# Kernel tuning notes

Hardware: AMD Instinct MI355X
Metric: run time of the kernel (lower is better)

Reference implementation:

```python
import jax, jax.numpy as jnp
import numpy as np

H = 16      # attention heads
D = 1024    # embedding size
HD = 64     # head size = D // H


def setup_inputs() -> dict:
    key = jax.random.key(0)
    ks = jax.random.split(key, 6)
    s = 1.0 / np.sqrt(D)
    x = jax.random.normal(ks[0], (2, 2048, D), dtype=jnp.float32)
    Wq = jax.random.normal(ks[1], (H, D, HD), dtype=jnp.float32) * s
    Wk = jax.random.normal(ks[2], (H, D, HD), dtype=jnp.float32) * s
    Wv = jax.random.normal(ks[3], (H, D, HD), dtype=jnp.float32) * s
    Wo = jax.random.normal(ks[4], (H * HD, D), dtype=jnp.float32) * s
    bo = jax.random.normal(ks[5], (D,), dtype=jnp.float32) * 0.01
    return {"x": x, "Wq": Wq, "Wk": Wk, "Wv": Wv, "Wo": Wo, "bo": bo}


def reference(x, Wq, Wk, Wv, Wo, bo):
    # x: [B, S, D]; per-head projections batched over the head axis.
    B, S, _ = x.shape
    q = jnp.einsum('bsd,hde->bhse', x, Wq)  # [B,H,S,HD]
    k = jnp.einsum('bsd,hde->bhse', x, Wk)
    v = jnp.einsum('bsd,hde->bhse', x, Wv)
    scale = 1.0 / jnp.sqrt(jnp.asarray(HD, dtype=x.dtype))
    scores = jnp.einsum('bhqe,bhke->bhqk', q, k) * scale  # [B,H,S,S]
    causal = jnp.tril(jnp.ones((S, S), dtype=bool))
    scores = jnp.where(causal, scores, jnp.asarray(-jnp.inf, dtype=x.dtype))
    attn = jax.nn.softmax(scores, axis=-1)
    out = jnp.einsum('bhqk,bhke->bhqe', attn, v)  # [B,H,S,HD]
    # concat heads along last dim (head order matches ModuleList order)
    out = out.transpose(0, 2, 1, 3).reshape(B, S, H * HD)
    return out @ Wo + bo  # dropout is identity in eval mode
```

## Files before the change

kernel.cpp:

```cpp
#include <hip/hip_runtime.h>
#include <hip/hip_bf16.h>
#include <cstdint>

#define Hh 16
#define Dd 1024
#define HD 64
#define Bb 2
#define Ss 2048

typedef float f32x4 __attribute__((ext_vector_type(4)));
typedef __bf16 bf16x8 __attribute__((ext_vector_type(8)));

__device__ __forceinline__ unsigned short f2bf(float f) {
  union { float f; unsigned u; } v; v.f = f;
  unsigned r = (v.u + 0x7FFFu + ((v.u >> 16) & 1u)) >> 16;
  return (unsigned short)r;
}

__device__ __forceinline__ void gld16(const void* g, void* l) {
  __builtin_amdgcn_global_load_lds(
      (__attribute__((address_space(1))) void*)(g),
      (__attribute__((address_space(3))) void*)(l),
      16, 0, 0);
}

__global__ __launch_bounds__(256)
void pack_x_k(const float4* __restrict__ x, unsigned short* __restrict__ xb, int n4) {
  const int i = blockIdx.x * blockDim.x + threadIdx.x;
  if (i >= n4) return;
  const float4 v = x[i];
  ushort4 o;
  o.x = f2bf(v.x); o.y = f2bf(v.y); o.z = f2bf(v.z); o.w = f2bf(v.w);
  *(ushort4*)&xb[(size_t)i * 4] = o;
}

__global__ __launch_bounds__(256)
void tconv_k(const float* __restrict__ in, unsigned short* __restrict__ out,
             int R, int C, float scale) {
  __shared__ float T[64][65];
  const int m = blockIdx.z;
  const float* src = in + (size_t)m * R * C;
  unsigned short* dst = out + (size_t)m * R * C;
  const int c0 = blockIdx.x * 64, r0 = blockIdx.y * 64;
  const int tx = threadIdx.x & 63, ty = threadIdx.x >> 6;
#pragma unroll
  for (int it = 0; it < 16; ++it) {
    const int i = ty + it * 4;
    T[i][tx] = src[(size_t)(r0 + i) * C + c0 + tx];
  }
  __syncthreads();
#pragma unroll
  for (int it = 0; it < 16; ++it) {
    const int jj = ty + it * 4;
    dst[(size_t)(c0 + jj) * R + r0 + tx] = f2bf(T[tx][jj] * scale);
  }
}

template <int EPI>
__global__ __launch_bounds__(256)
void gemm_bt(const unsigned short* __restrict__ A,
             const unsigned short* __restrict__ Bt,
             int K, int Ndim,
             unsigned short* __restrict__ q_out,
             unsigned short* __restrict__ k_out,
             unsigned short* __restrict__ vt_out,
             float* __restrict__ o_out,
             const float* __restrict__ bias)
{
  __shared__ unsigned short As[2][128 * 64];
  __shared__ unsigned short Bs[2][128 * 64];

  const int tid = threadIdx.x;
  const int w = tid >> 6, lane = tid & 63;
  const int lo = lane & 15, hi = lane >> 4;
  const int wr = w >> 1, wc = w & 1;
  const int row0 = blockIdx.y * 128;
  const int col0 = blockIdx.x * 128;

  f32x4 acc[4][4] = {};

  const int srow = w * 32 + (lane >> 3);
  const int scol = ((lane & 7) ^ (lane >> 3)) * 8;
  const int swl  = (lo & 7) << 4;

#define GSTAGE(bi, k0)                                                    \
  _Pragma("unroll")                                                       \
  for (int c = 0; c < 4; ++c) {                                           \
    const int rr = srow + c * 8;                                          \
    gld16(A  + (size_t)(row0 + rr) * K + ((k0) + scol),                   \
          (char*)&As[bi][0] + (w * 4 + c) * 1024);                        \
    gld16(Bt + (size_t)(col0 + rr) * K + ((k0) + scol),                   \
          (char*)&Bs[bi][0] + (w * 4 + c) * 1024);                        \
  }

  GSTAGE(0, 0);
  __syncthreads();

  const int nst = K >> 6;
  int cur = 0;
  for (int t = 0; t < nst; ++t) {
    if (t + 1 < nst) { GSTAGE(cur ^ 1, (t + 1) * 64); }
#pragma unroll
    for (int ks = 0; ks < 2; ++ks) {
      bf16x8 af[4], bfr[4];
#pragma unroll
      for (int i = 0; i < 4; ++i)
        af[i] = *(const bf16x8*)((const char*)&As[cur][0] +
                 (wr * 64 + i * 16 + lo) * 128 + ((ks * 64 + hi * 16) ^ swl));
#pragma unroll
      for (int j = 0; j < 4; ++j)
        bfr[j] = *(const bf16x8*)((const char*)&Bs[cur][0] +
                 (wc * 64 + j * 16 + lo) * 128 + ((ks * 64 + hi * 16) ^ swl));
      __builtin_amdgcn_s_setprio(1);
#pragma unroll
      for (int i = 0; i < 4; ++i)
#pragma unroll
        for (int j = 0; j < 4; ++j) {
          if (EPI == 1)
            acc[i][j] = __builtin_amdgcn_mfma_f32_16x16x32_bf16(af[i], bfr[j], acc[i][j], 0, 0, 0);
          else
            acc[i][j] = __builtin_amdgcn_mfma_f32_16x16x32_bf16(bfr[j], af[i], acc[i][j], 0, 0, 0);
        }
      __builtin_amdgcn_s_setprio(0);
    }
    __syncthreads();
    cur ^= 1;
  }

#pragma unroll
  for (int i = 0; i < 4; ++i) {
#pragma unroll
    for (int j = 0; j < 4; ++j) {
      if (EPI == 1) {
        const int grow = row0 + wr * 64 + i * 16 + hi * 4;
        const int gcol = col0 + wc * 64 + j * 16 + lo;
        const int hd = gcol >> 6, e = gcol & 63;
        const int bb2 = grow >> 11, s = grow & 2047;
        ushort4 pk;
        pk.x = f2bf(acc[i][j][0]); pk.y = f2bf(acc[i][j][1]);
        pk.z = f2bf(acc[i][j][2]); pk.w = f2bf(acc[i][j][3]);
        *(ushort4*)&vt_out[((size_t)(bb2 * Hh + hd) * HD + e) * Ss + s] = pk;
      } else {
        const int m  = row0 + wr * 64 + i * 16 + lo;
        const int n0 = col0 + wc * 64 + j * 16 + hi * 4;
        if (EPI == 0) {
          const int p = n0 >> 10;
          const int hd = (n0 >> 6) & 15;
          const int e = n0 & 63;
          const int bb2 = m >> 11, s = m & 2047;
          unsigned short* dst = (p == 0) ? q_out : k_out;
          ushort4 pk;
          pk.x = f2bf(acc[i][j][0]); pk.y = f2bf(acc[i][j][1]);
          pk.z = f2bf(acc[i][j][2]); pk.w = f2bf(acc[i][j][3]);
          *(ushort4*)&dst[((size_t)(bb2 * Hh + hd) * Ss + s) * HD + e] = pk;
        } else {
          const float4 bv = *(const float4*)&bias[n0];
          float4 o;
          o.x = acc[i][j][0] + bv.x; o.y = acc[i][j][1] + bv.y;
          o.z = acc[i][j][2] + bv.z; o.w = acc[i][j][3] + bv.w;
          *(float4*)&o_out[(size_t)m * Ndim + n0] = o;
        }
      }
    }
  }
#undef GSTAGE
}

__global__ __launch_bounds__(256)
void attn_fwd(const unsigned short* __restrict__ qb,
              const unsigned short* __restrict__ kb,
              const unsigned short* __restrict__ vtb,
              unsigned short* __restrict__ ob)
{
  __shared__ unsigned short Ks[2][64 * 64];
  __shared__ unsigned short Vs[2][64 * 64];
  __shared__ unsigned short Ps[4][16 * 64];

  const int qt = 31 - blockIdx.y;
  const int bh = blockIdx.x;
  const int bb2 = bh >> 4;
  const int hd = bh & 15;

  const unsigned short* Q  = qb  + (size_t)bh * Ss * HD;
  const unsigned short* Kg = kb  + (size_t)bh * Ss * HD;
  const unsigned short* Vt = vtb + (size_t)bh * HD * Ss;

  const int tid = threadIdx.x;
  const int w = tid >> 6, lane = tid & 63;
  const int lo = lane & 15, hi = lane >> 4;
  const int qrow0 = qt * 64 + w * 16;

  const int srow = lane >> 3;
  const int scol = ((lane & 7) ^ (lane >> 3)) * 8;

#define STAGE(bi, kv)                                                     \
  _Pragma("unroll")                                                       \
  for (int c = 0; c < 2; ++c) {                                           \
    const int L = c * 4 + w;                                              \
    const int rr = L * 8 + srow;                                          \
    gld16(Kg + (size_t)((kv) + rr) * HD + scol,                           \
          (char*)&Ks[bi][0] + L * 1024);                                  \
    gld16(Vt + (size_t)rr * Ss + (kv) + scol,                             \
          (char*)&Vs[bi][0] + L * 1024);                                  \
  }

  const int swl = (lo & 7) << 4;

  bf16x8 vones;
#pragma unroll
  for (int j = 0; j < 8; ++j) vones[j] = (__bf16)1.0f;

  bf16x8 qf[2];
#pragma unroll
  for (int ks = 0; ks < 2; ++ks)
    qf[ks] = *(const bf16x8*)&Q[(size_t)(qrow0 + lo) * HD + ks * 32 + hi * 8];

  f32x4 oacc[4] = {};
  float m2[4], l2[4];
#pragma unroll
  for (int r = 0; r < 4; ++r) { m2[r] = -INFINITY; l2[r] = 0.f; }

  const int ntiles = qt + 1;

  STAGE(0, 0);
  __syncthreads();

  int cur = 0;
  for (int t = 0; t < ntiles; ++t) {
    if (t + 1 < ntiles) { STAGE(cur ^ 1, (t + 1) * 64); }

    const int kv0 = t * 64;
    const bool diag = (t == qt);

    f32x4 sacc[4] = {};
    __builtin_amdgcn_s_setprio(1);
#pragma unroll
    for (int ks = 0; ks < 2; ++ks) {
      bf16x8 kf[4];
#pragma unroll
      for (int nj = 0; nj < 4; ++nj)
        kf[nj] = *(const bf16x8*)((const char*)&Ks[cur][0] +
                 (nj * 16 + lo) * 128 + ((ks * 64 + hi * 16) ^ swl));
#pragma unroll
      for (int nj = 0; nj < 4; ++nj)
        sacc[nj] = __builtin_amdgcn_mfma_f32_16x16x32_bf16(qf[ks], kf[nj], sacc[nj], 0, 0, 0);
    }
    __builtin_amdgcn_s_setprio(0);

    float lm[4];
    float dmax = -INFINITY;
#pragma unroll
    for (int r = 0; r < 4; ++r) {
      if (diag) {
        const int q = qrow0 + hi * 4 + r;
#pragma unroll
        for (int nj = 0; nj < 4; ++nj) {
          const int kk = kv0 + nj * 16 + lo;
          if (kk > q) sacc[nj][r] = -INFINITY;
        }
      }
      lm[r] = fmaxf(fmaxf(sacc[0][r], sacc[1][r]), fmaxf(sacc[2][r], sacc[3][r]));
      dmax = fmaxf(dmax, lm[r] - m2[r]);
    }
    if (!__all(dmax <= 8.0f)) {
#pragma unroll
      for (int r = 0; r < 4; ++r) {
        float rm = lm[r];
#pragma unroll
        for (int d = 1; d < 16; d <<= 1)
          rm = fmaxf(rm, __shfl_xor(rm, d, 64));
        const float mn = fmaxf(m2[r], rm);
        const float rc = __builtin_amdgcn_exp2f(m2[r] - mn);
        m2[r] = mn;
        l2[r] *= rc;
#pragma unroll
        for (int nj = 0; nj < 4; ++nj)
          oacc[nj][r] *= rc;
      }
    }

    unsigned short* Pw = &Ps[w][0];
#pragma unroll
    for (int nj = 0; nj < 4; ++nj)
#pragma unroll
      for (int r = 0; r < 4; ++r) {
        const float p = __builtin_amdgcn_exp2f(sacc[nj][r] - m2[r]);
        const int prow = hi * 4 + r;
        const int pcb = (nj * 32 + lo * 2) ^ ((prow & 7) << 4);
        *(__bf16*)((char*)Pw + prow * 128 + pcb) = (__bf16)p;
      }

    f32x4 osum = {};
    __builtin_amdgcn_s_setprio(1);
#pragma unroll
    for (int ks = 0; ks < 2; ++ks) {
      bf16x8 pa, vf[4];
      pa = *(const bf16x8*)((const char*)Pw +
           lo * 128 + ((ks * 64 + hi * 16) ^ swl));
#pragma unroll
      for (int nj = 0; nj < 4; ++nj)
        vf[nj] = *(const bf16x8*)((const char*)&Vs[cur][0] +
                 (nj * 16 + lo) * 128 + ((ks * 64 + hi * 16) ^ swl));
#pragma unroll
      for (int nj = 0; nj < 4; ++nj)
        oacc[nj] = __builtin_amdgcn_mfma_f32_16x16x32_bf16(pa, vf[nj], oacc[nj], 0, 0, 0);
      osum = __builtin_amdgcn_mfma_f32_16x16x32_bf16(pa, vones, osum, 0, 0, 0);
    }
    __builtin_amdgcn_s_setprio(0);
#pragma unroll
    for (int r = 0; r < 4; ++r)
      l2[r] += osum[r];

    __syncthreads();
    cur ^= 1;
  }
#undef STAGE

#pragma unroll
  for (int r = 0; r < 4; ++r) {
    const int s = qrow0 + hi * 4 + r;
    const float il = 1.0f / l2[r];
    const size_t base = ((size_t)bb2 * Ss + s) * Dd + hd * HD;
#pragma unroll
    for (int nj = 0; nj < 4; ++nj)
      ob[base + nj * 16 + lo] = f2bf(oacc[nj][r] * il);
  }
}

extern "C" void kernel_launch(void* const* d_in, const int* in_sizes, int n_in,
                              void* d_out, int out_size, void* d_ws, size_t ws_size,
                              hipStream_t stream)
{
  const float* x  = (const float*)d_in[0];
  const float* Wq = (const float*)d_in[1];
  const float* Wk = (const float*)d_in[2];
  const float* Wv = (const float*)d_in[3];
  const float* Wo = (const float*)d_in[4];
  const float* bo = (const float*)d_in[5];
  float* out = (float*)d_out;

  char* ws = (char*)d_ws;
  unsigned short* xb    = (unsigned short*)(ws);
  unsigned short* wqkvT = (unsigned short*)(ws + 8388608);
  unsigned short* woT   = (unsigned short*)(ws + 14680064);
  unsigned short* qb    = (unsigned short*)(ws + 16777216);
  unsigned short* kb    = (unsigned short*)(ws + 25165824);
  unsigned short* vtb   = (unsigned short*)(ws + 33554432);
  unsigned short* ob    = (unsigned short*)(ws + 41943040);

  pack_x_k<<<4096, 256, 0, stream>>>((const float4*)x, xb, 1048576);
  tconv_k<<<dim3(1, 16, 16), 256, 0, stream>>>(Wq, wqkvT,           1024, 64, 0.18033688011112042f);
  tconv_k<<<dim3(1, 16, 16), 256, 0, stream>>>(Wk, wqkvT + 1048576, 1024, 64, 1.0f);
  tconv_k<<<dim3(1, 16, 16), 256, 0, stream>>>(Wv, wqkvT + 2097152, 1024, 64, 1.0f);
  tconv_k<<<dim3(16, 16, 1), 256, 0, stream>>>(Wo, woT,             1024, 1024, 1.0f);

  gemm_bt<0><<<dim3(16, 32), 256, 0, stream>>>(xb, wqkvT, 1024, 0,
                                               qb, kb, nullptr, nullptr, nullptr);
  gemm_bt<1><<<dim3(8, 32), 256, 0, stream>>>(xb, wqkvT + 2097152, 1024, 0,
                                              nullptr, nullptr, vtb, nullptr, nullptr);
  attn_fwd<<<dim3(32, 32), 256, 0, stream>>>(qb, kb, vtb, ob);
  gemm_bt<2><<<dim3(8, 32), 256, 0, stream>>>(ob, woT, 1024, 1024,
                                              nullptr, nullptr, nullptr, out, bo);
}
```

Before: 131.0 us.

## Keep attention probabilities in registers and give each wave 32 query rows

```diff
diff --git a/kernel.cpp b/kernel.cpp
--- a/kernel.cpp
+++ b/kernel.cpp
@@ -166,7 +166,7 @@
 #undef GSTAGE
 }
 
-__global__ __launch_bounds__(256)
+__global__ __launch_bounds__(128)
 void attn_fwd(const unsigned short* __restrict__ qb,
               const unsigned short* __restrict__ kb,
               const unsigned short* __restrict__ vtb,
@@ -174,7 +174,6 @@
 {
   __shared__ unsigned short Ks[2][64 * 64];
   __shared__ unsigned short Vs[2][64 * 64];
-  __shared__ unsigned short Ps[4][16 * 64];
 
   const int qt = 31 - blockIdx.y;
   const int bh = blockIdx.x;
@@ -188,19 +187,24 @@
   const int tid = threadIdx.x;
   const int w = tid >> 6, lane = tid & 63;
   const int lo = lane & 15, hi = lane >> 4;
-  const int qrow0 = qt * 64 + w * 16;
-
-  const int srow = lane >> 3;
-  const int scol = ((lane & 7) ^ (lane >> 3)) * 8;
+  const int qrow0 = qt * 64 + w * 32;
+
+  const int sr  = lane >> 3;
+  const int scol = ((lane & 7) ^ sr) * 8;
+  int prow[4];
+#pragma unroll
+  for (int c = 0; c < 4; ++c) {
+    const int L = c * 2 + w;
+    prow[c] = (L >> 2) * 32 + ((L & 1) * 2 + (sr >> 2)) * 8 + ((L >> 1) & 1) * 4 + (sr & 3);
+  }
 
 #define STAGE(bi, kv)                                                     \
   _Pragma("unroll")                                                       \
-  for (int c = 0; c < 2; ++c) {                                           \
-    const int L = c * 4 + w;                                              \
-    const int rr = L * 8 + srow;                                          \
-    gld16(Kg + (size_t)((kv) + rr) * HD + scol,                           \
+  for (int c = 0; c < 4; ++c) {                                           \
+    const int L = c * 2 + w;                                              \
+    gld16(Kg + (size_t)((kv) + prow[c]) * HD + scol,                      \
           (char*)&Ks[bi][0] + L * 1024);                                  \
-    gld16(Vt + (size_t)rr * Ss + (kv) + scol,                             \
+    gld16(Vt + (size_t)(L * 8 + sr) * Ss + (kv) + scol,                   \
           (char*)&Vs[bi][0] + L * 1024);                                  \
   }
 
@@ -210,15 +214,22 @@
 #pragma unroll
   for (int j = 0; j < 8; ++j) vones[j] = (__bf16)1.0f;
 
-  bf16x8 qf[2];
-#pragma unroll
-  for (int ks = 0; ks < 2; ++ks)
-    qf[ks] = *(const bf16x8*)&Q[(size_t)(qrow0 + lo) * HD + ks * 32 + hi * 8];
-
-  f32x4 oacc[4] = {};
-  float m2[4], l2[4];
-#pragma unroll
-  for (int r = 0; r < 4; ++r) { m2[r] = -INFINITY; l2[r] = 0.f; }
+  bf16x8 qf[2][2];
+#pragma unroll
+  for (int mi = 0; mi < 2; ++mi)
+#pragma unroll
+    for (int ks = 0; ks < 2; ++ks)
+      qf[mi][ks] = *(const bf16x8*)&Q[(size_t)(qrow0 + mi * 16 + lo) * HD + ks * 32 + hi * 8];
+
+  f32x4 oacc[2][4] = {};
+  float m2s[2];
+  float l2[2][4];
+#pragma unroll
+  for (int mi = 0; mi < 2; ++mi) {
+    m2s[mi] = -INFINITY;
+#pragma unroll
+    for (int r = 0; r < 4; ++r) l2[mi][r] = 0.f;
+  }
 
   const int ntiles = qt + 1;
 
@@ -229,10 +240,7 @@
   for (int t = 0; t < ntiles; ++t) {
     if (t + 1 < ntiles) { STAGE(cur ^ 1, (t + 1) * 64); }
 
-    const int kv0 = t * 64;
-    const bool diag = (t == qt);
-
-    f32x4 sacc[4] = {};
+    f32x4 sacc[2][4] = {};
     __builtin_amdgcn_s_setprio(1);
 #pragma unroll
     for (int ks = 0; ks < 2; ++ks) {
@@ -242,74 +250,98 @@
         kf[nj] = *(const bf16x8*)((const char*)&Ks[cur][0] +
                  (nj * 16 + lo) * 128 + ((ks * 64 + hi * 16) ^ swl));
 #pragma unroll
-      for (int nj = 0; nj < 4; ++nj)
-        sacc[nj] = __builtin_amdgcn_mfma_f32_16x16x32_bf16(qf[ks], kf[nj], sacc[nj], 0, 0, 0);
+      for (int mi = 0; mi < 2; ++mi)
+#pragma unroll
+        for (int nj = 0; nj < 4; ++nj)
+          sacc[mi][nj] = __builtin_amdgcn_mfma_f32_16x16x32_bf16(kf[nj], qf[mi][ks], sacc[mi][nj], 0, 0, 0);
     }
     __builtin_amdgcn_s_setprio(0);
 
-    float lm[4];
-    float dmax = -INFINITY;
-#pragma unroll
-    for (int r = 0; r < 4; ++r) {
-      if (diag) {
-        const int q = qrow0 + hi * 4 + r;
+    if (t == qt) {
+#pragma unroll
+      for (int mi = 0; mi < 2; ++mi) {
+        const int qr = w * 32 + mi * 16 + lo;
 #pragma unroll
         for (int nj = 0; nj < 4; ++nj) {
-          const int kk = kv0 + nj * 16 + lo;
-          if (kk > q) sacc[nj][r] = -INFINITY;
+          const int kb0 = (nj >> 1) * 32 + (nj & 1) * 4 + hi * 8;
+#pragma unroll
+          for (int r = 0; r < 4; ++r)
+            if (kb0 + r > qr) sacc[mi][nj][r] = -INFINITY;
         }
       }
-      lm[r] = fmaxf(fmaxf(sacc[0][r], sacc[1][r]), fmaxf(sacc[2][r], sacc[3][r]));
-      dmax = fmaxf(dmax, lm[r] - m2[r]);
-    }
+    }
+
+    float lmax[2];
+#pragma unroll
+    for (int mi = 0; mi < 2; ++mi) {
+      float a = fmaxf(fmaxf(sacc[mi][0][0], sacc[mi][0][1]),
+                      fmaxf(sacc[mi][0][2], sacc[mi][0][3]));
+      float b = fmaxf(fmaxf(sacc[mi][1][0], sacc[mi][1][1]),
+                      fmaxf(sacc[mi][1][2], sacc[mi][1][3]));
+      float c = fmaxf(fmaxf(sacc[mi][2][0], sacc[mi][2][1]),
+                      fmaxf(sacc[mi][2][2], sacc[mi][2][3]));
+      float d = fmaxf(fmaxf(sacc[mi][3][0], sacc[mi][3][1]),
+                      fmaxf(sacc[mi][3][2], sacc[mi][3][3]));
+      lmax[mi] = fmaxf(fmaxf(a, b), fmaxf(c, d));
+    }
+    const float dmax = fmaxf(lmax[0] - m2s[0], lmax[1] - m2s[1]);
     if (!__all(dmax <= 8.0f)) {
-#pragma unroll
-      for (int r = 0; r < 4; ++r) {
-        float rm = lm[r];
-#pragma unroll
-        for (int d = 1; d < 16; d <<= 1)
-          rm = fmaxf(rm, __shfl_xor(rm, d, 64));
-        const float mn = fmaxf(m2[r], rm);
-        const float rc = __builtin_amdgcn_exp2f(m2[r] - mn);
-        m2[r] = mn;
-        l2[r] *= rc;
-#pragma unroll
-        for (int nj = 0; nj < 4; ++nj)
-          oacc[nj][r] *= rc;
+      float rcs[2];
+#pragma unroll
+      for (int mi = 0; mi < 2; ++mi) {
+        float rm = lmax[mi];
+        rm = fmaxf(rm, __shfl_xor(rm, 16, 64));
+        rm = fmaxf(rm, __shfl_xor(rm, 32, 64));
+        const float mn = fmaxf(m2s[mi], rm);
+        rcs[mi] = __builtin_amdgcn_exp2f(m2s[mi] - mn);
+        m2s[mi] = mn;
       }
-    }
-
-    unsigned short* Pw = &Ps[w][0];
-#pragma unroll
-    for (int nj = 0; nj < 4; ++nj)
-#pragma unroll
-      for (int r = 0; r < 4; ++r) {
-        const float p = __builtin_amdgcn_exp2f(sacc[nj][r] - m2[r]);
-        const int prow = hi * 4 + r;
-        const int pcb = (nj * 32 + lo * 2) ^ ((prow & 7) << 4);
-        *(__bf16*)((char*)Pw + prow * 128 + pcb) = (__bf16)p;
-      }
-
-    f32x4 osum = {};
+#pragma unroll
+      for (int mi = 0; mi < 2; ++mi)
+#pragma unroll
+        for (int r = 0; r < 4; ++r) {
+          const float rc = __shfl(rcs[mi], hi * 4 + r, 64);
+          l2[mi][r] *= rc;
+#pragma unroll
+          for (int nj = 0; nj < 4; ++nj)
+            oacc[mi][nj][r] *= rc;
+        }
+    }
+
+    bf16x8 pa[2][2];
+#pragma unroll
+    for (int mi = 0; mi < 2; ++mi)
+#pragma unroll
+      for (int ks = 0; ks < 2; ++ks)
+#pragma unroll
+        for (int j = 0; j < 4; ++j) {
+          pa[mi][ks][j]     = (__bf16)__builtin_amdgcn_exp2f(sacc[mi][2 * ks][j]     - m2s[mi]);
+          pa[mi][ks][4 + j] = (__bf16)__builtin_amdgcn_exp2f(sacc[mi][2 * ks + 1][j] - m2s[mi]);
+        }
+
+    f32x4 osum[2] = {};
     __builtin_amdgcn_s_setprio(1);
 #pragma unroll
     for (int ks = 0; ks < 2; ++ks) {
-      bf16x8 pa, vf[4];
-      pa = *(const bf16x8*)((const char*)Pw +
-           lo * 128 + ((ks * 64 + hi * 16) ^ swl));
+      bf16x8 vf[4];
 #pragma unroll
       for (int nj = 0; nj < 4; ++nj)
         vf[nj] = *(const bf16x8*)((const char*)&Vs[cur][0] +
                  (nj * 16 + lo) * 128 + ((ks * 64 + hi * 16) ^ swl));
 #pragma unroll
-      for (int nj = 0; nj < 4; ++nj)
-        oacc[nj] = __builtin_amdgcn_mfma_f32_16x16x32_bf16(pa, vf[nj], oacc[nj], 0, 0, 0);
-      osum = __builtin_amdgcn_mfma_f32_16x16x32_bf16(pa, vones, osum, 0, 0, 0);
+      for (int mi = 0; mi < 2; ++mi) {
+#pragma unroll
+        for (int nj = 0; nj < 4; ++nj)
+          oacc[mi][nj] = __builtin_amdgcn_mfma_f32_16x16x32_bf16(pa[mi][ks], vf[nj], oacc[mi][nj], 0, 0, 0);
+        osum[mi] = __builtin_amdgcn_mfma_f32_16x16x32_bf16(pa[mi][ks], vones, osum[mi], 0, 0, 0);
+      }
     }
     __builtin_amdgcn_s_setprio(0);
 #pragma unroll
-    for (int r = 0; r < 4; ++r)
-      l2[r] += osum[r];
+    for (int mi = 0; mi < 2; ++mi)
+#pragma unroll
+      for (int r = 0; r < 4; ++r)
+        l2[mi][r] += osum[mi][r];
 
     __syncthreads();
     cur ^= 1;
@@ -317,13 +349,16 @@
 #undef STAGE
 
 #pragma unroll
-  for (int r = 0; r < 4; ++r) {
-    const int s = qrow0 + hi * 4 + r;
-    const float il = 1.0f / l2[r];
-    const size_t base = ((size_t)bb2 * Ss + s) * Dd + hd * HD;
-#pragma unroll
-    for (int nj = 0; nj < 4; ++nj)
-      ob[base + nj * 16 + lo] = f2bf(oacc[nj][r] * il);
+  for (int mi = 0; mi < 2; ++mi) {
+#pragma unroll
+    for (int r = 0; r < 4; ++r) {
+      const int s = qrow0 + mi * 16 + hi * 4 + r;
+      const float il = 1.0f / l2[mi][r];
+      const size_t base = ((size_t)bb2 * Ss + s) * Dd + hd * HD;
+#pragma unroll
+      for (int nj = 0; nj < 4; ++nj)
+        ob[base + nj * 16 + lo] = f2bf(oacc[mi][nj][r] * il);
+    }
   }
 }
 
@@ -358,7 +393,7 @@
                                                qb, kb, nullptr, nullptr, nullptr);
   gemm_bt<1><<<dim3(8, 32), 256, 0, stream>>>(xb, wqkvT + 2097152, 1024, 0,
                                               nullptr, nullptr, vtb, nullptr, nullptr);
-  attn_fwd<<<dim3(32, 32), 256, 0, stream>>>(qb, kb, vtb, ob);
+  attn_fwd<<<dim3(32, 32), 128, 0, stream>>>(qb, kb, vtb, ob);
   gemm_bt<2><<<dim3(8, 32), 256, 0, stream>>>(ob, woT, 1024, 1024,
                                               nullptr, nullptr, nullptr, out, bo);
 }
```

Result: slower. 135.3 us (+3.2%).

## Merge QKV GEMMs into one launch and keep attention probabilities in registers

Applied to the files above, without the earlier changes.

```diff
diff --git a/kernel.cpp b/kernel.cpp
--- a/kernel.cpp
+++ b/kernel.cpp
@@ -56,26 +56,24 @@
   }
 }
 
-template <int EPI>
 __global__ __launch_bounds__(256)
-void gemm_bt(const unsigned short* __restrict__ A,
-             const unsigned short* __restrict__ Bt,
-             int K, int Ndim,
-             unsigned short* __restrict__ q_out,
-             unsigned short* __restrict__ k_out,
-             unsigned short* __restrict__ vt_out,
-             float* __restrict__ o_out,
-             const float* __restrict__ bias)
+void gemm_qkv(const unsigned short* __restrict__ A,
+              const unsigned short* __restrict__ Bt,
+              unsigned short* __restrict__ q_out,
+              unsigned short* __restrict__ k_out,
+              unsigned short* __restrict__ vt_out)
 {
   __shared__ unsigned short As[2][128 * 64];
   __shared__ unsigned short Bs[2][128 * 64];
 
+  const int K = 1024;
   const int tid = threadIdx.x;
   const int w = tid >> 6, lane = tid & 63;
   const int lo = lane & 15, hi = lane >> 4;
   const int wr = w >> 1, wc = w & 1;
   const int row0 = blockIdx.y * 128;
   const int col0 = blockIdx.x * 128;
+  const bool isv = (col0 >= 2048);
 
   f32x4 acc[4][4] = {};
 
@@ -96,10 +94,9 @@
   GSTAGE(0, 0);
   __syncthreads();
 
-  const int nst = K >> 6;
   int cur = 0;
-  for (int t = 0; t < nst; ++t) {
-    if (t + 1 < nst) { GSTAGE(cur ^ 1, (t + 1) * 64); }
+  for (int t = 0; t < 16; ++t) {
+    if (t + 1 < 16) { GSTAGE(cur ^ 1, (t + 1) * 64); }
 #pragma unroll
     for (int ks = 0; ks < 2; ++ks) {
       bf16x8 af[4], bfr[4];
@@ -112,15 +109,19 @@
         bfr[j] = *(const bf16x8*)((const char*)&Bs[cur][0] +
                  (wc * 64 + j * 16 + lo) * 128 + ((ks * 64 + hi * 16) ^ swl));
       __builtin_amdgcn_s_setprio(1);
-#pragma unroll
-      for (int i = 0; i < 4; ++i)
-#pragma unroll
-        for (int j = 0; j < 4; ++j) {
-          if (EPI == 1)
+      if (isv) {
+#pragma unroll
+        for (int i = 0; i < 4; ++i)
+#pragma unroll
+          for (int j = 0; j < 4; ++j)
             acc[i][j] = __builtin_amdgcn_mfma_f32_16x16x32_bf16(af[i], bfr[j], acc[i][j], 0, 0, 0);
-          else
+      } else {
+#pragma unroll
+        for (int i = 0; i < 4; ++i)
+#pragma unroll
+          for (int j = 0; j < 4; ++j)
             acc[i][j] = __builtin_amdgcn_mfma_f32_16x16x32_bf16(bfr[j], af[i], acc[i][j], 0, 0, 0);
-        }
+      }
       __builtin_amdgcn_s_setprio(0);
     }
     __syncthreads();
@@ -131,10 +132,10 @@
   for (int i = 0; i < 4; ++i) {
 #pragma unroll
     for (int j = 0; j < 4; ++j) {
-      if (EPI == 1) {
+      if (isv) {
         const int grow = row0 + wr * 64 + i * 16 + hi * 4;
         const int gcol = col0 + wc * 64 + j * 16 + lo;
-        const int hd = gcol >> 6, e = gcol & 63;
+        const int hd = (gcol >> 6) & 15, e = gcol & 63;
         const int bb2 = grow >> 11, s = grow & 2047;
         ushort4 pk;
         pk.x = f2bf(acc[i][j][0]); pk.y = f2bf(acc[i][j][1]);
@@ -143,24 +144,93 @@
       } else {
         const int m  = row0 + wr * 64 + i * 16 + lo;
         const int n0 = col0 + wc * 64 + j * 16 + hi * 4;
-        if (EPI == 0) {
-          const int p = n0 >> 10;
-          const int hd = (n0 >> 6) & 15;
-          const int e = n0 & 63;
-          const int bb2 = m >> 11, s = m & 2047;
-          unsigned short* dst = (p == 0) ? q_out : k_out;
-          ushort4 pk;
-          pk.x = f2bf(acc[i][j][0]); pk.y = f2bf(acc[i][j][1]);
-          pk.z = f2bf(acc[i][j][2]); pk.w = f2bf(acc[i][j][3]);
-          *(ushort4*)&dst[((size_t)(bb2 * Hh + hd) * Ss + s) * HD + e] = pk;
-        } else {
-          const float4 bv = *(const float4*)&bias[n0];
-          float4 o;
-          o.x = acc[i][j][0] + bv.x; o.y = acc[i][j][1] + bv.y;
-          o.z = acc[i][j][2] + bv.z; o.w = acc[i][j][3] + bv.w;
-          *(float4*)&o_out[(size_t)m * Ndim + n0] = o;
-        }
+        const int p = n0 >> 10;
+        const int hd = (n0 >> 6) & 15, e = n0 & 63;
+        const int bb2 = m >> 11, s = m & 2047;
+        unsigned short* dst = (p == 0) ? q_out : k_out;
+        ushort4 pk;
+        pk.x = f2bf(acc[i][j][0]); pk.y = f2bf(acc[i][j][1]);
+        pk.z = f2bf(acc[i][j][2]); pk.w = f2bf(acc[i][j][3]);
+        *(ushort4*)&dst[((size_t)(bb2 * Hh + hd) * Ss + s) * HD + e] = pk;
       }
+    }
+  }
+#undef GSTAGE
+}
+
+__global__ __launch_bounds__(256)
+void gemm_out(const unsigned short* __restrict__ A,
+              const unsigned short* __restrict__ Bt,
+              float* __restrict__ o_out,
+              const float* __restrict__ bias)
+{
+  __shared__ unsigned short As[2][128 * 64];
+  __shared__ unsigned short Bs[2][128 * 64];
+
+  const int K = 1024, Ndim = 1024;
+  const int tid = threadIdx.x;
+  const int w = tid >> 6, lane = tid & 63;
+  const int lo = lane & 15, hi = lane >> 4;
+  const int wr = w >> 1, wc = w & 1;
+  const int row0 = blockIdx.y * 128;
+  const int col0 = blockIdx.x * 128;
+
+  f32x4 acc[4][4] = {};
+
+  const int srow = w * 32 + (lane >> 3);
+  const int scol = ((lane & 7) ^ (lane >> 3)) * 8;
+  const int swl  = (lo & 7) << 4;
+
+#define GSTAGE(bi, k0)                                                    \
+  _Pragma("unroll")                                                       \
+  for (int c = 0; c < 4; ++c) {                                           \
+    const int rr = srow + c * 8;                                          \
+    gld16(A  + (size_t)(row0 + rr) * K + ((k0) + scol),                   \
+          (char*)&As[bi][0] + (w * 4 + c) * 1024);                        \
+    gld16(Bt + (size_t)(col0 + rr) * K + ((k0) + scol),                   \
+          (char*)&Bs[bi][0] + (w * 4 + c) * 1024);                        \
+  }
+
+  GSTAGE(0, 0);
+  __syncthreads();
+
+  int cur = 0;
+  for (int t = 0; t < 16; ++t) {
+    if (t + 1 < 16) { GSTAGE(cur ^ 1, (t + 1) * 64); }
+#pragma unroll
+    for (int ks = 0; ks < 2; ++ks) {
+      bf16x8 af[4], bfr[4];
+#pragma unroll
+      for (int i = 0; i < 4; ++i)
+        af[i] = *(const bf16x8*)((const char*)&As[cur][0] +
+                 (wr * 64 + i * 16 + lo) * 128 + ((ks * 64 + hi * 16) ^ swl));
+#pragma unroll
+      for (int j = 0; j < 4; ++j)
+        bfr[j] = *(const bf16x8*)((const char*)&Bs[cur][0] +
+                 (wc * 64 + j * 16 + lo) * 128 + ((ks * 64 + hi * 16) ^ swl));
+      __builtin_amdgcn_s_setprio(1);
+#pragma unroll
+      for (int i = 0; i < 4; ++i)
+#pragma unroll
+        for (int j = 0; j < 4; ++j)
+          acc[i][j] = __builtin_amdgcn_mfma_f32_16x16x32_bf16(bfr[j], af[i], acc[i][j], 0, 0, 0);
+      __builtin_amdgcn_s_setprio(0);
+    }
+    __syncthreads();
+    cur ^= 1;
+  }
+
+#pragma unroll
+  for (int i = 0; i < 4; ++i) {
+#pragma unroll
+    for (int j = 0; j < 4; ++j) {
+      const int m  = row0 + wr * 64 + i * 16 + lo;
+      const int n0 = col0 + wc * 64 + j * 16 + hi * 4;
+      const float4 bv = *(const float4*)&bias[n0];
+      float4 o;
+      o.x = acc[i][j][0] + bv.x; o.y = acc[i][j][1] + bv.y;
+      o.z = acc[i][j][2] + bv.z; o.w = acc[i][j][3] + bv.w;
+      *(float4*)&o_out[(size_t)m * Ndim + n0] = o;
     }
   }
 #undef GSTAGE
@@ -174,7 +244,6 @@
 {
   __shared__ unsigned short Ks[2][64 * 64];
   __shared__ unsigned short Vs[2][64 * 64];
-  __shared__ unsigned short Ps[4][16 * 64];
 
   const int qt = 31 - blockIdx.y;
   const int bh = blockIdx.x;
@@ -190,17 +259,22 @@
   const int lo = lane & 15, hi = lane >> 4;
   const int qrow0 = qt * 64 + w * 16;
 
-  const int srow = lane >> 3;
-  const int scol = ((lane & 7) ^ (lane >> 3)) * 8;
+  const int sr   = lane >> 3;
+  const int scol = ((lane & 7) ^ sr) * 8;
+  int prow[2];
+#pragma unroll
+  for (int c = 0; c < 2; ++c) {
+    const int L = c * 4 + w;
+    prow[c] = (L >> 2) * 32 + ((L & 1) * 2 + (sr >> 2)) * 8 + ((L >> 1) & 1) * 4 + (sr & 3);
+  }
 
 #define STAGE(bi, kv)                                                     \
   _Pragma("unroll")                                                       \
   for (int c = 0; c < 2; ++c) {                                           \
     const int L = c * 4 + w;                                              \
-    const int rr = L * 8 + srow;                                          \
-    gld16(Kg + (size_t)((kv) + rr) * HD + scol,                           \
+    gld16(Kg + (size_t)((kv) + prow[c]) * HD + scol,                      \
           (char*)&Ks[bi][0] + L * 1024);                                  \
-    gld16(Vt + (size_t)rr * Ss + (kv) + scol,                             \
+    gld16(Vt + (size_t)(L * 8 + sr) * Ss + (kv) + scol,                   \
           (char*)&Vs[bi][0] + L * 1024);                                  \
   }
 
@@ -216,9 +290,10 @@
     qf[ks] = *(const bf16x8*)&Q[(size_t)(qrow0 + lo) * HD + ks * 32 + hi * 8];
 
   f32x4 oacc[4] = {};
-  float m2[4], l2[4];
-#pragma unroll
-  for (int r = 0; r < 4; ++r) { m2[r] = -INFINITY; l2[r] = 0.f; }
+  float m2s = -INFINITY;
+  float l2[4];
+#pragma unroll
+  for (int r = 0; r < 4; ++r) l2[r] = 0.f;
 
   const int ntiles = qt + 1;
 
@@ -229,9 +304,6 @@
   for (int t = 0; t < ntiles; ++t) {
     if (t + 1 < ntiles) { STAGE(cur ^ 1, (t + 1) * 64); }
 
-    const int kv0 = t * 64;
-    const bool diag = (t == qt);
-
     f32x4 sacc[4] = {};
     __builtin_amdgcn_s_setprio(1);
 #pragma unroll
@@ -243,35 +315,36 @@
                  (nj * 16 + lo) * 128 + ((ks * 64 + hi * 16) ^ swl));
 #pragma unroll
       for (int nj = 0; nj < 4; ++nj)
-        sacc[nj] = __builtin_amdgcn_mfma_f32_16x16x32_bf16(qf[ks], kf[nj], sacc[nj], 0, 0, 0);
+        sacc[nj] = __builtin_amdgcn_mfma_f32_16x16x32_bf16(kf[nj], qf[ks], sacc[nj], 0, 0, 0);
     }
     __builtin_amdgcn_s_setprio(0);
 
-    float lm[4];
-    float dmax = -INFINITY;
-#pragma unroll
-    for (int r = 0; r < 4; ++r) {
-      if (diag) {
-        const int q = qrow0 + hi * 4 + r;
-#pragma unroll
-        for (int nj = 0; nj < 4; ++nj) {
-          const int kk = kv0 + nj * 16 + lo;
-          if (kk > q) sacc[nj][r] = -INFINITY;
-        }
+    if (t == qt) {
+      const int qr = w * 16 + lo;
+#pragma unroll
+      for (int nj = 0; nj < 4; ++nj) {
+        const int kb0 = (nj >> 1) * 32 + (nj & 1) * 4 + hi * 8;
+#pragma unroll
+        for (int r = 0; r < 4; ++r)
+          if (kb0 + r > qr) sacc[nj][r] = -INFINITY;
       }
-      lm[r] = fmaxf(fmaxf(sacc[0][r], sacc[1][r]), fmaxf(sacc[2][r], sacc[3][r]));
-      dmax = fmaxf(dmax, lm[r] - m2[r]);
-    }
-    if (!__all(dmax <= 8.0f)) {
+    }
+
+    float a0 = fmaxf(fmaxf(sacc[0][0], sacc[0][1]), fmaxf(sacc[0][2], sacc[0][3]));
+    float a1 = fmaxf(fmaxf(sacc[1][0], sacc[1][1]), fmaxf(sacc[1][2], sacc[1][3]));
+    float a2 = fmaxf(fmaxf(sacc[2][0], sacc[2][1]), fmaxf(sacc[2][2], sacc[2][3]));
+    float a3 = fmaxf(fmaxf(sacc[3][0], sacc[3][1]), fmaxf(sacc[3][2], sacc[3][3]));
+    const float lmax = fmaxf(fmaxf(a0, a1), fmaxf(a2, a3));
+    if (!__all(lmax - m2s <= 8.0f)) {
+      float rm = lmax;
+      rm = fmaxf(rm, __shfl_xor(rm, 16, 64));
+      rm = fmaxf(rm, __shfl_xor(rm, 32, 64));
+      const float mn = fmaxf(m2s, rm);
+      const float rcs = __builtin_amdgcn_exp2f(m2s - mn);
+      m2s = mn;
 #pragma unroll
       for (int r = 0; r < 4; ++r) {
-        float rm = lm[r];
-#pragma unroll
-        for (int d = 1; d < 16; d <<= 1)
-          rm = fmaxf(rm, __shfl_xor(rm, d, 64));
-        const float mn = fmaxf(m2[r], rm);
-        const float rc = __builtin_amdgcn_exp2f(m2[r] - mn);
-        m2[r] = mn;
+        const float rc = __shfl(rcs, hi * 4 + r, 64);
         l2[r] *= rc;
 #pragma unroll
         for (int nj = 0; nj < 4; ++nj)
@@ -279,32 +352,28 @@
       }
     }
 
-    unsigned short* Pw = &Ps[w][0];
-#pragma unroll
-    for (int nj = 0; nj < 4; ++nj)
-#pragma unroll
-      for (int r = 0; r < 4; ++r) {
-        const float p = __builtin_amdgcn_exp2f(sacc[nj][r] - m2[r]);
-        const int prow = hi * 4 + r;
-        const int pcb = (nj * 32 + lo * 2) ^ ((prow & 7) << 4);
-        *(__bf16*)((char*)Pw + prow * 128 + pcb) = (__bf16)p;
+    bf16x8 pa[2];
+#pragma unroll
+    for (int ks = 0; ks < 2; ++ks)
+#pragma unroll
+      for (int j = 0; j < 4; ++j) {
+        pa[ks][j]     = (__bf16)__builtin_amdgcn_exp2f(sacc[2 * ks][j]     - m2s);
+        pa[ks][4 + j] = (__bf16)__builtin_amdgcn_exp2f(sacc[2 * ks + 1][j] - m2s);
       }
 
     f32x4 osum = {};
     __builtin_amdgcn_s_setprio(1);
 #pragma unroll
     for (int ks = 0; ks < 2; ++ks) {
-      bf16x8 pa, vf[4];
-      pa = *(const bf16x8*)((const char*)Pw +
-           lo * 128 + ((ks * 64 + hi * 16) ^ swl));
+      bf16x8 vf[4];
 #pragma unroll
       for (int nj = 0; nj < 4; ++nj)
         vf[nj] = *(const bf16x8*)((const char*)&Vs[cur][0] +
                  (nj * 16 + lo) * 128 + ((ks * 64 + hi * 16) ^ swl));
 #pragma unroll
       for (int nj = 0; nj < 4; ++nj)
-        oacc[nj] = __builtin_amdgcn_mfma_f32_16x16x32_bf16(pa, vf[nj], oacc[nj], 0, 0, 0);
-      osum = __builtin_amdgcn_mfma_f32_16x16x32_bf16(pa, vones, osum, 0, 0, 0);
+        oacc[nj] = __builtin_amdgcn_mfma_f32_16x16x32_bf16(pa[ks], vf[nj], oacc[nj], 0, 0, 0);
+      osum = __builtin_amdgcn_mfma_f32_16x16x32_bf16(pa[ks], vones, osum, 0, 0, 0);
     }
     __builtin_amdgcn_s_setprio(0);
 #pragma unroll
@@ -354,11 +423,7 @@
   tconv_k<<<dim3(1, 16, 16), 256, 0, stream>>>(Wv, wqkvT + 2097152, 1024, 64, 1.0f);
   tconv_k<<<dim3(16, 16, 1), 256, 0, stream>>>(Wo, woT,             1024, 1024, 1.0f);
 
-  gemm_bt<0><<<dim3(16, 32), 256, 0, stream>>>(xb, wqkvT, 1024, 0,
-                                               qb, kb, nullptr, nullptr, nullptr);
-  gemm_bt<1><<<dim3(8, 32), 256, 0, stream>>>(xb, wqkvT + 2097152, 1024, 0,
-                                              nullptr, nullptr, vtb, nullptr, nullptr);
+  gemm_qkv<<<dim3(24, 32), 256, 0, stream>>>(xb, wqkvT, qb, kb, vtb);
   attn_fwd<<<dim3(32, 32), 256, 0, stream>>>(qb, kb, vtb, ob);
-  gemm_bt<2><<<dim3(8, 32), 256, 0, stream>>>(ob, woT, 1024, 1024,
-                                              nullptr, nullptr, nullptr, out, bo);
-}
+  gemm_out<<<dim3(8, 32), 256, 0, stream>>>(ob, woT, out, bo);
+}
```

New measurement: 131.8 us. No clear change (+0.6%).
